# Kernel optimization log

Hardware: AMD Instinct MI355X
Metric: run time of the kernel (lower is better)

## Reference

```python
import jax, jax.numpy as jnp
import numpy as np

N_NODES, N_EDGES, D_IN, N_GRAPHS = 20000, 320000, 256, 32
H1, C1, H2, C2 = 4, 128, 4, 64


def setup_inputs() -> dict:
    key = jax.random.key(0)
    ks = jax.random.split(key, 24)
    g = lambda k, shape, fan: jax.random.normal(k, shape, jnp.float32) * (1.0 / np.sqrt(fan))
    inp = {
        'x': jax.random.normal(ks[0], (N_NODES, D_IN), jnp.float32),
        'edge_index': jax.random.randint(ks[1], (2, N_EDGES), 0, N_NODES, jnp.int32),
        'batch': jnp.sort(jax.random.randint(ks[2], (N_NODES,), 0, N_GRAPHS, jnp.int32)),
        'edge_attr': jax.random.normal(ks[3], (N_EDGES, 1), jnp.float32),
        # GATConv 1: lin [D_IN, H1*C1], att_src/dst/edge [H1,C1], lin_edge [1,H1*C1], bias [H1*C1]
        'W1': g(ks[4], (D_IN, H1 * C1), D_IN),
        'as1': g(ks[5], (H1, C1), C1),
        'ad1': g(ks[6], (H1, C1), C1),
        'We1': g(ks[7], (1, H1 * C1), 1),
        'ae1': g(ks[8], (H1, C1), C1),
        'b1': jnp.zeros((H1 * C1,), jnp.float32),
        'g1': jnp.ones((H1 * C1,), jnp.float32),
        'be1': jnp.zeros((H1 * C1,), jnp.float32),
        # GATConv 2 (concat=False -> out 64)
        'W2': g(ks[9], (H1 * C1, H2 * C2), H1 * C1),
        'as2': g(ks[10], (H2, C2), C2),
        'ad2': g(ks[11], (H2, C2), C2),
        'We2': g(ks[12], (1, H2 * C2), 1),
        'ae2': g(ks[13], (H2, C2), C2),
        'b2': jnp.zeros((C2,), jnp.float32),
        'g2': jnp.ones((C2,), jnp.float32),
        'be2': jnp.zeros((C2,), jnp.float32),
        'fw1': g(ks[14], (C2, 32), C2),
        'fb1': jnp.zeros((32,), jnp.float32),
        'fw2': g(ks[15], (32, 1), 32),
        'fb2': jnp.zeros((1,), jnp.float32),
    }
    return inp


def _gat(x, src, dst, ea, W, a_s, a_d, We, a_e, bias, H, C, concat, n):
    h = (x @ W).reshape(n, H, C)                         # [N,H,C]
    al_s = jnp.einsum('nhc,hc->nh', h, a_s)              # [N,H]
    al_d = jnp.einsum('nhc,hc->nh', h, a_d)
    e = (ea @ We).reshape(-1, H, C)                      # [E',H,C]
    al_e = jnp.einsum('ehc,hc->eh', e, a_e)
    logits = jax.nn.leaky_relu(al_s[src] + al_d[dst] + al_e, 0.2)  # [E',H]
    m = jax.ops.segment_max(logits, dst, num_segments=n)
    m = jnp.where(jnp.isfinite(m), m, 0.0)
    p = jnp.exp(logits - m[dst])
    denom = jax.ops.segment_sum(p, dst, num_segments=n)
    alpha = p / (denom[dst] + 1e-16)                     # segment softmax
    out = jax.ops.segment_sum(h[src] * alpha[:, :, None], dst, num_segments=n)
    out = out.reshape(n, H * C) if concat else out.mean(axis=1)
    return out + bias


def _bn(x, gamma, beta):
    mu = x.mean(axis=0)
    var = x.var(axis=0)
    return gamma * (x - mu) * jax.lax.rsqrt(var + 1e-5) + beta


def reference(x, edge_index, batch, edge_attr, W1, as1, ad1, We1, ae1, b1, g1, be1,
              W2, as2, ad2, We2, ae2, b2, g2, be2, fw1, fb1, fw2, fb2):
    n = x.shape[0]
    loop = jnp.arange(n, dtype=edge_index.dtype)
    src = jnp.concatenate([edge_index[0], loop])
    dst = jnp.concatenate([edge_index[1], loop])
    # self-loop edge_attr filled with mean (PyG fill_value='mean')
    ea = jnp.concatenate([edge_attr, jnp.broadcast_to(edge_attr.mean(axis=0), (n, edge_attr.shape[1]))])

    h = _gat(x, src, dst, ea, W1, as1, ad1, We1, ae1, b1, H1, C1, True, n)
    h = jax.nn.elu(_bn(h, g1, be1))
    h = _gat(h, src, dst, ea, W2, as2, ad2, We2, ae2, b2, H2, C2, False, n)
    h = jax.nn.elu(_bn(h, g2, be2))

    sums = jax.ops.segment_sum(h, batch, num_segments=N_GRAPHS)
    cnt = jax.ops.segment_sum(jnp.ones((n,), h.dtype), batch, num_segments=N_GRAPHS)
    pooled = sums / jnp.maximum(cnt, 1.0)[:, None]       # global_mean_pool
    # dropout is identity in eval mode
    out = jax.nn.elu(pooled @ fw1 + fb1) @ fw2 + fb2
    return out
```

## Files before the change

### kernel.cpp

```cpp
#include <hip/hip_runtime.h>
#include <hip/hip_bf16.h>

#define N_NODES  20000
#define MPAD     20096
#define N_EDGES  320000
#define N_EP     (N_EDGES + N_NODES)
#define D_IN     256
#define N_GRAPHS 32
#define HH1 4
#define CC1 128
#define HH2 4
#define CC2 64
#define MAXDEG   128

#define XB_OFF      0ull
#define HB1_OFF     10289152ull
#define AGG1_OFF    30867456ull
#define HB2_OFF     51445760ull
#define OUT2_OFF    61734912ull
#define EAF_OFF     66854912ull
#define W1BT_OFF    68134912ull
#define W2BT_OFF    68397056ull
#define CSR_OFF     68659200ull
#define ROWPTR_OFF  71379200ull
#define GSTART_OFF  71459264ull
#define SMALL_OFF   71459520ull
#define SBUF_OFF    71485120ull
#define EAP_OFF     71485184ull
#define ALSP_OFF    71486464ull
#define ALDP_OFF    72129536ull
#define PMU1_OFF    72772608ull
#define PM21_OFF    73296896ull
#define PMU2_OFF    73821184ull
#define PM22_OFF    73886720ull
#define A1_OFF      73952256ull
#define B1_OFF      73954304ull
#define A2_OFF      73956352ull
#define B2_OFF      73956608ull
#define EAACC_OFF   73956864ull
#define ALS_OFF     73956928ull
#define ALD_OFF     74278464ull
#define DEG_OFF     74600000ull
#define CURS_OFF    74680000ull
#define FLAGZ_OFF   74760000ull
#define ZERO0_START DEG_OFF
#define ZERO0_SIZE  160128ull
#define PP_OFF      74760128ull

#define S_AS1 0
#define S_AD1 512
#define S_WE1 1024
#define S_AE1 1536
#define S_G1  2048
#define S_BE1 2560
#define S_AS2 3072
#define S_AD2 3328
#define S_WE2 3584
#define S_AE2 3840
#define S_G2  4096
#define S_BE2 4160
#define S_FW1 4224
#define S_FB1 6272
#define S_FW2 6304
#define S_FB2 6336

typedef __attribute__((ext_vector_type(8))) short bf8_t;
typedef __attribute__((ext_vector_type(4))) float f4_t;

__global__ void detect_dtype(const unsigned short* __restrict__ xr, int* __restrict__ flag) {
    int i = blockIdx.x * blockDim.x + threadIdx.x;
    unsigned short u = xr[i];
    if ((u & 0x7F80) == 0x7F80) atomicOr(flag, 1);
}

__device__ __forceinline__ float loadF(const void* p, int i, int fp32) {
    return fp32 ? ((const float*)p)[i]
                : __bfloat162float(((const __hip_bfloat16*)p)[i]);
}

#define PB_XB  5024
#define PB_EAF 313
#define PB_W   512
#define PB_SM  16
#define PREP_BLOCKS (PB_XB + PB_EAF + 2 * PB_W + PB_SM + 1)
__global__ __launch_bounds__(256) void prep(
        const int* __restrict__ flag,
        const void* x, const void* ea, const void* W1, const void* W2,
        const void* as1, const void* ad1, const void* We1, const void* ae1,
        const void* g1, const void* be1, const void* as2, const void* ad2,
        const void* We2, const void* ae2, const void* g2, const void* be2,
        const void* fw1, const void* fb1, const void* fw2, const void* fb2,
        __hip_bfloat16* __restrict__ xb, float* __restrict__ eaf, float* __restrict__ eap,
        __hip_bfloat16* __restrict__ W1bt, __hip_bfloat16* __restrict__ W2bt,
        float* __restrict__ smalls, float* __restrict__ sbuf) {
    __shared__ float sh[256];
    int b = blockIdx.x, t = threadIdx.x;
    int fp32 = flag[0];
    if (b < PB_XB) {
        int base = (b * 256 + t) * 4;
        __hip_bfloat16 tmp[4];
#pragma unroll
        for (int j = 0; j < 4; ++j) {
            int i = base + j;
            float v = (i < N_NODES * D_IN) ? loadF(x, i, fp32) : 0.f;
            tmp[j] = __float2bfloat16(v);
        }
        *(uint2*)&xb[base] = *(uint2*)tmp;
        return;
    }
    b -= PB_XB;
    if (b < PB_EAF) {
        int base = (b * 256 + t) * 4;
        float s = 0.f;
#pragma unroll
        for (int j = 0; j < 4; ++j) {
            int i = base + j;
            if (i < N_EDGES) { float v = loadF(ea, i, fp32); eaf[i] = v; s += v; }
        }
        sh[t] = s;
        __syncthreads();
        for (int st = 128; st; st >>= 1) {
            if (t < st) sh[t] += sh[t + st];
            __syncthreads();
        }
        if (t == 0) eap[b] = sh[0];
        return;
    }
    b -= PB_EAF;
    if (b < PB_W) {
        int i = b * 256 + t;
        int k = i >> 9, n = i & 511;
        W1bt[(size_t)n * 256 + k] = __float2bfloat16(loadF(W1, i, fp32));
        return;
    }
    b -= PB_W;
    if (b < PB_W) {
        int i = b * 256 + t;
        int k = i >> 8, n = i & 255;
        W2bt[(size_t)n * 512 + k] = __float2bfloat16(loadF(W2, i, fp32));
        return;
    }
    b -= PB_W;
    if (b < PB_SM) {
        const void* srcs[16] = {as1, ad1, We1, ae1, g1, be1, as2, ad2, We2, ae2, g2, be2, fw1, fb1, fw2, fb2};
        const int cnts[16] = {512, 512, 512, 512, 512, 512, 256, 256, 256, 256, 64, 64, 2048, 32, 32, 1};
        const int offs[16] = {S_AS1, S_AD1, S_WE1, S_AE1, S_G1, S_BE1, S_AS2, S_AD2,
                              S_WE2, S_AE2, S_G2, S_BE2, S_FW1, S_FB1, S_FW2, S_FB2};
        for (int i = t; i < cnts[b]; i += 256)
            smalls[offs[b] + i] = loadF(srcs[b], i, fp32);
        return;
    }
    if (t < 4) {
        float s = 0.f;
        for (int c = 0; c < CC1; ++c) s += loadF(We1, t * CC1 + c, fp32) * loadF(ae1, t * CC1 + c, fp32);
        sbuf[t] = s;
    } else if (t < 8) {
        int h = t - 4;
        float s = 0.f;
        for (int c = 0; c < CC2; ++c) s += loadF(We2, h * CC2 + c, fp32) * loadF(ae2, h * CC2 + c, fp32);
        sbuf[4 + h] = s;
    }
}

#define HIST_BLOCKS 1329
__global__ void hist_bounds(const int* __restrict__ ei, int* __restrict__ deg,
                            const int* __restrict__ batch, int* __restrict__ gstart) {
    int b = blockIdx.x, t = threadIdx.x;
    if (b < HIST_BLOCKS) {
        int e = b * 256 + t;
        if (e >= N_EP) return;
        int d = (e < N_EDGES) ? ei[N_EDGES + e] : e - N_EDGES;
        atomicAdd(&deg[d], 1);
        return;
    }
    int i = (b - HIST_BLOCKS) * 256 + t;
    if (i >= N_NODES) return;
    int bb = batch[i];
    if (i == 0) {
        for (int g = 0; g <= bb; ++g) gstart[g] = 0;
    } else {
        int pb = batch[i - 1];
        for (int g = pb + 1; g <= bb; ++g) gstart[g] = i;
    }
    if (i == N_NODES - 1) {
        for (int g = bb + 1; g <= N_GRAPHS; ++g) gstart[g] = N_NODES;
    }
}

__global__ __launch_bounds__(1024) void deg_scan(const int* __restrict__ deg, int* __restrict__ rowptr,
                                                 const float* __restrict__ eap, float* __restrict__ ea_acc) {
    __shared__ int part[1024];
    int t = threadIdx.x;
    int lo = t * 20;
    int hi = lo + 20; if (hi > N_NODES) hi = N_NODES; if (lo > N_NODES) lo = N_NODES;
    int s = 0;
    for (int i = lo; i < hi; ++i) s += deg[i];
    part[t] = s;
    __syncthreads();
    for (int off = 1; off < 1024; off <<= 1) {
        int u = (t >= off) ? part[t - off] : 0;
        __syncthreads();
        if (t >= off) part[t] += u;
        __syncthreads();
    }
    int run = part[t] - s;
    for (int i = lo; i < hi; ++i) { rowptr[i] = run; run += deg[i]; }
    if (hi == N_NODES && lo < N_NODES) rowptr[N_NODES] = run;
    if (t == 0) {
        float es = 0.f;
        for (int i = 0; i < PB_EAF; ++i) es += eap[i];
        ea_acc[0] = es;
    }
}

__global__ void edge_scatter(const int* __restrict__ ei, const int* __restrict__ rowptr,
                             int* __restrict__ cursor, int2* __restrict__ csr_se) {
    int e = blockIdx.x * blockDim.x + threadIdx.x;
    if (e >= N_EP) return;
    int s, d;
    if (e < N_EDGES) { s = ei[e]; d = ei[N_EDGES + e]; }
    else { s = d = e - N_EDGES; }
    int pos = rowptr[d] + atomicAdd(&cursor[d], 1);
    csr_se[pos] = make_int2(s, e);
}

__global__ __launch_bounds__(64) void csr_sort(const int* __restrict__ rowptr, int2* __restrict__ cs) {
    __shared__ int2 buf[128];
    int d = blockIdx.x;
    int beg = rowptr[d], end = rowptr[d + 1], n = end - beg;
    int lane = threadIdx.x;
    if (n <= 1) return;
    if (n <= 128) {
        for (int i = lane; i < n; i += 64) buf[i] = cs[beg + i];
        __syncthreads();
        if (lane == 0) {
            for (int i = 1; i < n; ++i) {
                int2 key = buf[i]; int j = i - 1;
                while (j >= 0 && buf[j].y > key.y) { buf[j + 1] = buf[j]; --j; }
                buf[j + 1] = key;
            }
        }
        __syncthreads();
        for (int i = lane; i < n; i += 64) cs[beg + i] = buf[i];
    } else if (lane == 0) {
        for (int i = beg + 1; i < end; ++i) {
            int2 key = cs[i]; int j = i - 1;
            while (j >= beg && cs[j].y > key.y) { cs[j + 1] = cs[j]; --j; }
            cs[j + 1] = key;
        }
    }
}

__global__ __launch_bounds__(256) void gemm_mfma_al(
        const short* __restrict__ A, const short* __restrict__ Bt,
        __hip_bfloat16* __restrict__ Cb, int N, int K,
        float* __restrict__ alsp, float* __restrict__ aldp,
        const float* __restrict__ asv, const float* __restrict__ adv, int cshift) {
    __shared__ short As[128 * 40];
    __shared__ short Bs[64 * 40];
    int t = threadIdx.x;
    int wv = t >> 6, lane = t & 63, quad = lane >> 4, lr = lane & 15;
    int m0 = blockIdx.y * 128, n0 = blockIdx.x * 64;
    f4_t acc[2][4] = {};
    int ra0 = t >> 2, sa0 = t & 3;
    int ra1 = (t + 256) >> 2;
    for (int k0 = 0; k0 < K; k0 += 32) {
        *(uint4*)&As[ra0 * 40 + sa0 * 8] = *(const uint4*)&A[(size_t)(m0 + ra0) * K + k0 + sa0 * 8];
        *(uint4*)&As[ra1 * 40 + sa0 * 8] = *(const uint4*)&A[(size_t)(m0 + ra1) * K + k0 + sa0 * 8];
        *(uint4*)&Bs[ra0 * 40 + sa0 * 8] = *(const uint4*)&Bt[(size_t)(n0 + ra0) * K + k0 + sa0 * 8];
        __syncthreads();
        bf8_t a0 = *(const bf8_t*)&As[(wv * 16 + lr) * 40 + quad * 8];
        bf8_t a1 = *(const bf8_t*)&As[((wv + 4) * 16 + lr) * 40 + quad * 8];
#pragma unroll
        for (int nt = 0; nt < 4; ++nt) {
            bf8_t b = *(const bf8_t*)&Bs[(nt * 16 + lr) * 40 + quad * 8];
            acc[0][nt] = __builtin_amdgcn_mfma_f32_16x16x32_bf16(a0, b, acc[0][nt], 0, 0, 0);
            acc[1][nt] = __builtin_amdgcn_mfma_f32_16x16x32_bf16(a1, b, acc[1][nt], 0, 0, 0);
        }
        __syncthreads();
    }
#pragma unroll
    for (int si = 0; si < 2; ++si) {
        int mrow = m0 + (wv + si * 4) * 16 + quad * 4;
#pragma unroll
        for (int nt = 0; nt < 4; ++nt) {
            int col = n0 + nt * 16 + lr;
#pragma unroll
            for (int r = 0; r < 4; ++r)
                Cb[(size_t)(mrow + r) * N + col] = __float2bfloat16(acc[si][nt][r]);
        }
    }
    float asv4[4], adv4[4];
#pragma unroll
    for (int nt = 0; nt < 4; ++nt) {
        asv4[nt] = asv[n0 + nt * 16 + lr];
        adv4[nt] = adv[n0 + nt * 16 + lr];
    }
    int hsel = n0 >> cshift;
    int parity = (n0 >> 6) & ((1 << (cshift - 6)) - 1);
#pragma unroll
    for (int si = 0; si < 2; ++si) {
#pragma unroll
        for (int r = 0; r < 4; ++r) {
            float ps = 0.f, pd = 0.f;
#pragma unroll
            for (int nt = 0; nt < 4; ++nt) {
                ps += acc[si][nt][r] * asv4[nt];
                pd += acc[si][nt][r] * adv4[nt];
            }
#pragma unroll
            for (int m = 1; m < 16; m <<= 1) {
                ps += __shfl_xor(ps, m);
                pd += __shfl_xor(pd, m);
            }
            if (lr == 0) {
                int row = m0 + (wv + si * 4) * 16 + quad * 4 + r;
                alsp[(row * 4 + hsel) * 2 + parity] = ps;
                aldp[(row * 4 + hsel) * 2 + parity] = pd;
            }
        }
    }
}

__global__ void al_combine(const float* __restrict__ alsp, const float* __restrict__ aldp,
                           float* __restrict__ als, float* __restrict__ ald, int nparts) {
    int i = blockIdx.x * blockDim.x + threadIdx.x;
    if (i >= MPAD * 4) return;
    float s = alsp[2 * i], d0 = aldp[2 * i];
    if (nparts == 2) { s += alsp[2 * i + 1]; d0 += aldp[2 * i + 1]; }
    als[i] = s; ald[i] = d0;
}

__global__ __launch_bounds__(128) void fused_agg1(
        const int* __restrict__ rowptr, const int2* __restrict__ cs,
        const float* __restrict__ als, const float* __restrict__ ald,
        const float* __restrict__ eaf, const float* __restrict__ ea_acc,
        const float* __restrict__ sbuf, const __hip_bfloat16* __restrict__ hb,
        __hip_bfloat16* __restrict__ outb) {
    __shared__ float lg[MAXDEG * 4];
    __shared__ int   ssrc[MAXDEG];
    __shared__ float red[4 * 128];
    __shared__ float mxs[4], dns[4];
    int d = blockIdx.x, t = threadIdx.x;
    int beg = rowptr[d], end = rowptr[d + 1], n = end - beg;
    bool fit = (n <= MAXDEG);
    float ea_mean = ea_acc[0] * (1.0f / N_EDGES);
    float4 adv = *(const float4*)&ald[d * 4];
    float adh[4] = {adv.x, adv.y, adv.z, adv.w};
    float sb[4] = {sbuf[0], sbuf[1], sbuf[2], sbuf[3]};
    float mx[4] = {-INFINITY, -INFINITY, -INFINITY, -INFINITY};
    for (int p = t; p < n; p += 128) {
        int2 se = cs[beg + p];
        float eav = (se.y < N_EDGES) ? eaf[se.y] : ea_mean;
        float4 as = *(const float4*)&als[se.x * 4];
        float as4[4] = {as.x, as.y, as.z, as.w};
#pragma unroll
        for (int h = 0; h < 4; ++h) {
            float l = as4[h] + adh[h] + eav * sb[h];
            l = l > 0.f ? l : 0.2f * l;
            if (fit) lg[p * 4 + h] = l;
            mx[h] = fmaxf(mx[h], l);
        }
        if (fit) ssrc[p] = se.x;
    }
#pragma unroll
    for (int i = 0; i < 4; ++i) red[i * 128 + t] = mx[i];
    __syncthreads();
    for (int s = 64; s; s >>= 1) {
        if (t < s) {
#pragma unroll
            for (int i = 0; i < 4; ++i)
                red[i * 128 + t] = fmaxf(red[i * 128 + t], red[i * 128 + t + s]);
        }
        __syncthreads();
    }
    if (t < 4) mxs[t] = red[t * 128];
    __syncthreads();
    float m4[4] = {mxs[0], mxs[1], mxs[2], mxs[3]};
    float sm[4] = {0.f, 0.f, 0.f, 0.f};
    if (fit) {
        for (int p = t; p < n; p += 128) {
            float4 lv = *(float4*)&lg[p * 4];
            lv.x = __expf(lv.x - m4[0]); lv.y = __expf(lv.y - m4[1]);
            lv.z = __expf(lv.z - m4[2]); lv.w = __expf(lv.w - m4[3]);
            *(float4*)&lg[p * 4] = lv;
            sm[0] += lv.x; sm[1] += lv.y; sm[2] += lv.z; sm[3] += lv.w;
        }
    } else {
        for (int p = t; p < n; p += 128) {
            int2 se = cs[beg + p];
            float eav = (se.y < N_EDGES) ? eaf[se.y] : ea_mean;
            float4 as = *(const float4*)&als[se.x * 4];
            float as4[4] = {as.x, as.y, as.z, as.w};
#pragma unroll
            for (int h = 0; h < 4; ++h) {
                float l = as4[h] + adh[h] + eav * sb[h];
                l = l > 0.f ? l : 0.2f * l;
                sm[h] += __expf(l - m4[h]);
            }
        }
    }
    __syncthreads();
#pragma unroll
    for (int i = 0; i < 4; ++i) red[i * 128 + t] = sm[i];
    __syncthreads();
    for (int s = 64; s; s >>= 1) {
        if (t < s) {
#pragma unroll
            for (int i = 0; i < 4; ++i)
                red[i * 128 + t] += red[i * 128 + t + s];
        }
        __syncthreads();
    }
    if (t < 4) dns[t] = red[t * 128];
    __syncthreads();
    int h = t >> 5;
    float rdn = 1.0f / (dns[h] + 1e-16f);
    float a0 = 0.f, a1 = 0.f, a2 = 0.f, a3 = 0.f;
    if (fit) {
        for (int p = 0; p < n; ++p) {
            float w = lg[p * 4 + h];
            uint2 raw = *(const uint2*)&hb[(size_t)ssrc[p] * 512 + 4 * t];
            a0 += w * __uint_as_float(raw.x << 16);
            a1 += w * __uint_as_float(raw.x & 0xFFFF0000u);
            a2 += w * __uint_as_float(raw.y << 16);
            a3 += w * __uint_as_float(raw.y & 0xFFFF0000u);
        }
    } else {
        for (int p = 0; p < n; ++p) {
            int2 se = cs[beg + p];
            float eav = (se.y < N_EDGES) ? eaf[se.y] : ea_mean;
            float l = als[se.x * 4 + h] + adh[h] + eav * sb[h];
            l = l > 0.f ? l : 0.2f * l;
            float w = __expf(l - m4[h]);
            uint2 raw = *(const uint2*)&hb[(size_t)se.x * 512 + 4 * t];
            a0 += w * __uint_as_float(raw.x << 16);
            a1 += w * __uint_as_float(raw.x & 0xFFFF0000u);
            a2 += w * __uint_as_float(raw.y << 16);
            a3 += w * __uint_as_float(raw.y & 0xFFFF0000u);
        }
    }
    __hip_bfloat16 tmp[4] = {__float2bfloat16(a0 * rdn), __float2bfloat16(a1 * rdn),
                             __float2bfloat16(a2 * rdn), __float2bfloat16(a3 * rdn)};
    *(uint2*)&outb[(size_t)d * 512 + 4 * t] = *(uint2*)tmp;
}

__global__ __launch_bounds__(64) void fused_agg2(
        const int* __restrict__ rowptr, const int2* __restrict__ cs,
        const float* __restrict__ als, const float* __restrict__ ald,
        const float* __restrict__ eaf, const float* __restrict__ ea_acc,
        const float* __restrict__ sbuf, const __hip_bfloat16* __restrict__ hb,
        float* __restrict__ out2) {
    __shared__ float lg[MAXDEG * 4];
    __shared__ int   ssrc[MAXDEG];
    __shared__ float red[4 * 64];
    __shared__ float mxs[4], dns[4];
    __shared__ float shm[256];
    int d = blockIdx.x, t = threadIdx.x;
    int beg = rowptr[d], end = rowptr[d + 1], n = end - beg;
    bool fit = (n <= MAXDEG);
    float ea_mean = ea_acc[0] * (1.0f / N_EDGES);
    float4 adv = *(const float4*)&ald[d * 4];
    float adh[4] = {adv.x, adv.y, adv.z, adv.w};
    float sb[4] = {sbuf[4], sbuf[5], sbuf[6], sbuf[7]};
    float mx[4] = {-INFINITY, -INFINITY, -INFINITY, -INFINITY};
    for (int p = t; p < n; p += 64) {
        int2 se = cs[beg + p];
        float eav = (se.y < N_EDGES) ? eaf[se.y] : ea_mean;
        float4 as = *(const float4*)&als[se.x * 4];
        float as4[4] = {as.x, as.y, as.z, as.w};
#pragma unroll
        for (int h = 0; h < 4; ++h) {
            float l = as4[h] + adh[h] + eav * sb[h];
            l = l > 0.f ? l : 0.2f * l;
            if (fit) lg[p * 4 + h] = l;
            mx[h] = fmaxf(mx[h], l);
        }
        if (fit) ssrc[p] = se.x;
    }
#pragma unroll
    for (int i = 0; i < 4; ++i) red[i * 64 + t] = mx[i];
    __syncthreads();
    for (int s = 32; s; s >>= 1) {
        if (t < s) {
#pragma unroll
            for (int i = 0; i < 4; ++i)
                red[i * 64 + t] = fmaxf(red[i * 64 + t], red[i * 64 + t + s]);
        }
        __syncthreads();
    }
    if (t < 4) mxs[t] = red[t * 64];
    __syncthreads();
    float m4[4] = {mxs[0], mxs[1], mxs[2], mxs[3]};
    float sm[4] = {0.f, 0.f, 0.f, 0.f};
    if (fit) {
        for (int p = t; p < n; p += 64) {
            float4 lv = *(float4*)&lg[p * 4];
            lv.x = __expf(lv.x - m4[0]); lv.y = __expf(lv.y - m4[1]);
            lv.z = __expf(lv.z - m4[2]); lv.w = __expf(lv.w - m4[3]);
            *(float4*)&lg[p * 4] = lv;
            sm[0] += lv.x; sm[1] += lv.y; sm[2] += lv.z; sm[3] += lv.w;
        }
    } else {
        for (int p = t; p < n; p += 64) {
            int2 se = cs[beg + p];
            float eav = (se.y < N_EDGES) ? eaf[se.y] : ea_mean;
            float4 as = *(const float4*)&als[se.x * 4];
            float as4[4] = {as.x, as.y, as.z, as.w};
#pragma unroll
            for (int h = 0; h < 4; ++h) {
                float l = as4[h] + adh[h] + eav * sb[h];
                l = l > 0.f ? l : 0.2f * l;
                sm[h] += __expf(l - m4[h]);
            }
        }
    }
    __syncthreads();
#pragma unroll
    for (int i = 0; i < 4; ++i) red[i * 64 + t] = sm[i];
    __syncthreads();
    for (int s = 32; s; s >>= 1) {
        if (t < s) {
#pragma unroll
            for (int i = 0; i < 4; ++i)
                red[i * 64 + t] += red[i * 64 + t + s];
        }
        __syncthreads();
    }
    if (t < 4) dns[t] = red[t * 64];
    __syncthreads();
    int h = t >> 4;
    float rdn = 1.0f / (dns[h] + 1e-16f);
    float a0 = 0.f, a1 = 0.f, a2 = 0.f, a3 = 0.f;
    if (fit) {
        for (int p = 0; p < n; ++p) {
            float w = lg[p * 4 + h];
            uint2 raw = *(const uint2*)&hb[(size_t)ssrc[p] * 256 + 4 * t];
            a0 += w * __uint_as_float(raw.x << 16);
            a1 += w * __uint_as_float(raw.x & 0xFFFF0000u);
            a2 += w * __uint_as_float(raw.y << 16);
            a3 += w * __uint_as_float(raw.y & 0xFFFF0000u);
        }
    } else {
        for (int p = 0; p < n; ++p) {
            int2 se = cs[beg + p];
            float eav = (se.y < N_EDGES) ? eaf[se.y] : ea_mean;
            float l = als[se.x * 4 + h] + adh[h] + eav * sb[h];
            l = l > 0.f ? l : 0.2f * l;
            float w = __expf(l - m4[h]);
            uint2 raw = *(const uint2*)&hb[(size_t)se.x * 256 + 4 * t];
            a0 += w * __uint_as_float(raw.x << 16);
            a1 += w * __uint_as_float(raw.x & 0xFFFF0000u);
            a2 += w * __uint_as_float(raw.y << 16);
            a3 += w * __uint_as_float(raw.y & 0xFFFF0000u);
        }
    }
    shm[4 * t] = a0 * rdn; shm[4 * t + 1] = a1 * rdn;
    shm[4 * t + 2] = a2 * rdn; shm[4 * t + 3] = a3 * rdn;
    __syncthreads();
    if (t < 16) {
        float4 v;
        v.x = 0.25f * (shm[4 * t] + shm[64 + 4 * t] + shm[128 + 4 * t] + shm[192 + 4 * t]);
        v.y = 0.25f * (shm[4 * t + 1] + shm[64 + 4 * t + 1] + shm[128 + 4 * t + 1] + shm[192 + 4 * t + 1]);
        v.z = 0.25f * (shm[4 * t + 2] + shm[64 + 4 * t + 2] + shm[128 + 4 * t + 2] + shm[192 + 4 * t + 2]);
        v.w = 0.25f * (shm[4 * t + 3] + shm[64 + 4 * t + 3] + shm[128 + 4 * t + 3] + shm[192 + 4 * t + 3]);
        *(float4*)&out2[(size_t)d * 64 + 4 * t] = v;
    }
}

__global__ __launch_bounds__(256) void bn_part_b(const __hip_bfloat16* __restrict__ x,
                                                 float* __restrict__ pmu, float* __restrict__ pm2) {
    int t = threadIdx.x, b = blockIdx.x;
    float s0 = 0.f, s20 = 0.f, s1 = 0.f, s21 = 0.f;
    for (int i = b; i < N_NODES; i += gridDim.x) {
        unsigned u = *(const unsigned*)&x[(size_t)i * 512 + 2 * t];
        float v0 = __uint_as_float(u << 16);
        float v1 = __uint_as_float(u & 0xFFFF0000u);
        s0 += v0; s20 += v0 * v0; s1 += v1; s21 += v1 * v1;
    }
    pmu[b * 512 + 2 * t] = s0;     pm2[b * 512 + 2 * t] = s20;
    pmu[b * 512 + 2 * t + 1] = s1; pm2[b * 512 + 2 * t + 1] = s21;
}

__global__ void bn_reduce_affine(const float* __restrict__ pmu, const float* __restrict__ pm2,
                                 const float* __restrict__ smalls, int s_g, int s_be,
                                 float* __restrict__ a, float* __restrict__ b, int nch) {
    int c = blockIdx.x * blockDim.x + threadIdx.x;
    if (c >= nch) return;
    float s = 0.f, s2 = 0.f;
    for (int bk = 0; bk < 256; ++bk) { s += pmu[bk * nch + c]; s2 += pm2[bk * nch + c]; }
    float m = s * (1.0f / N_NODES);
    float var = s2 * (1.0f / N_NODES) - m * m;
    float aa = smalls[s_g + c] * rsqrtf(var + 1e-5f);
    a[c] = aa;
    b[c] = smalls[s_be + c] - m * aa;
}

__global__ __launch_bounds__(256) void bn_apply_elu_b16(__hip_bfloat16* __restrict__ x,
                                                        const float* __restrict__ a,
                                                        const float* __restrict__ b) {
    int q = blockIdx.x * blockDim.x + threadIdx.x;
    if (q >= N_NODES * 512 / 4) return;
    int base = q * 4;
    int j = base & 511;
    uint2 raw = *(uint2*)&x[base];
    float v[4] = {__uint_as_float(raw.x << 16), __uint_as_float(raw.x & 0xFFFF0000u),
                  __uint_as_float(raw.y << 16), __uint_as_float(raw.y & 0xFFFF0000u)};
    __hip_bfloat16 tmp[4];
#pragma unroll
    for (int k = 0; k < 4; ++k) {
        float y = a[j + k] * v[k] + b[j + k];
        y = y > 0.f ? y : expm1f(y);
        tmp[k] = __float2bfloat16(y);
    }
    *(uint2*)&x[base] = *(uint2*)tmp;
}

__global__ __launch_bounds__(256) void bn2_stats(const float* __restrict__ x,
                                                 float* __restrict__ pmu, float* __restrict__ pm2) {
    int t = threadIdx.x;
    int c = t & 63, j = t >> 6;
    float ls = 0.f, ls2 = 0.f;
    for (int nd = blockIdx.x * 4 + j; nd < N_NODES; nd += gridDim.x * 4) {
        float v = x[(size_t)nd * 64 + c];
        ls += v; ls2 += v * v;
    }
    __shared__ float shs[4][64], sh2[4][64];
    shs[j][c] = ls; sh2[j][c] = ls2;
    __syncthreads();
    if (j == 0) {
        pmu[blockIdx.x * 64 + c] = shs[0][c] + shs[1][c] + shs[2][c] + shs[3][c];
        pm2[blockIdx.x * 64 + c] = sh2[0][c] + sh2[1][c] + sh2[2][c] + sh2[3][c];
    }
}

__global__ __launch_bounds__(256) void pool_part(const float* __restrict__ x, const int* __restrict__ gstart,
                                                 const float* __restrict__ a2, const float* __restrict__ b2,
                                                 float* __restrict__ pp) {
    int g = blockIdx.x >> 3, ck = blockIdx.x & 7;
    int t = threadIdx.x;
    int c = t & 63, j = t >> 6;
    int beg = gstart[g], end = gstart[g + 1], n = end - beg;
    int cb = beg + (n * ck) / 8, ce = beg + (n * (ck + 1)) / 8;
    float ac = a2[c], bc = b2[c];
    float s = 0.f;
    for (int i = cb + j; i < ce; i += 4) {
        float y = ac * x[(size_t)i * 64 + c] + bc;
        s += (y > 0.f ? y : expm1f(y));
    }
    __shared__ float sh[4][64];
    sh[j][c] = s;
    __syncthreads();
    if (j == 0)
        pp[blockIdx.x * 64 + c] = sh[0][c] + sh[1][c] + sh[2][c] + sh[3][c];
}

__global__ __launch_bounds__(64) void pool_mlp_fin(const float* __restrict__ pp, const int* __restrict__ gstart,
                                                   const float* __restrict__ smalls, const int* __restrict__ flag,
                                                   void* __restrict__ outp) {
    int g = blockIdx.x, t = threadIdx.x;
    __shared__ float pooled[64];
    __shared__ float hsh[32];
    float s = 0.f;
    for (int k = 0; k < 8; ++k) s += pp[(g * 8 + k) * 64 + t];
    int n = gstart[g + 1] - gstart[g];
    pooled[t] = s / fmaxf((float)n, 1.0f);
    __syncthreads();
    if (t < 32) {
        float acc = smalls[S_FB1 + t];
        for (int cc = 0; cc < 64; ++cc)
            acc += pooled[cc] * smalls[S_FW1 + cc * 32 + t];
        hsh[t] = acc > 0.f ? acc : expm1f(acc);
    }
    __syncthreads();
    if (t == 0) {
        float o = smalls[S_FB2];
        for (int k = 0; k < 32; ++k) o += hsh[k] * smalls[S_FW2 + k];
        if (flag[0]) ((float*)outp)[g] = o;
        else ((__hip_bfloat16*)outp)[g] = __float2bfloat16(o);
    }
}

extern "C" void kernel_launch(void* const* d_in, const int* in_sizes, int n_in,
                              void* d_out, int out_size, void* d_ws, size_t ws_size,
                              hipStream_t stream) {
    const void* x    = d_in[0];
    const int* ei    = (const int*)d_in[1];
    const int* batch = (const int*)d_in[2];
    const void* ea   = d_in[3];
    const void* W1   = d_in[4];
    const void* as1  = d_in[5];
    const void* ad1  = d_in[6];
    const void* We1  = d_in[7];
    const void* ae1  = d_in[8];
    const void* g1   = d_in[10];
    const void* be1  = d_in[11];
    const void* W2   = d_in[12];
    const void* as2  = d_in[13];
    const void* ad2  = d_in[14];
    const void* We2  = d_in[15];
    const void* ae2  = d_in[16];
    const void* g2   = d_in[18];
    const void* be2  = d_in[19];
    const void* fw1  = d_in[20];
    const void* fb1  = d_in[21];
    const void* fw2  = d_in[22];
    const void* fb2  = d_in[23];

    char* ws = (char*)d_ws;
    __hip_bfloat16* xb   = (__hip_bfloat16*)(ws + XB_OFF);
    __hip_bfloat16* hb1  = (__hip_bfloat16*)(ws + HB1_OFF);
    __hip_bfloat16* agg1 = (__hip_bfloat16*)(ws + AGG1_OFF);
    __hip_bfloat16* hb2  = (__hip_bfloat16*)(ws + HB2_OFF);
    float* out2   = (float*)(ws + OUT2_OFF);
    float* eaf    = (float*)(ws + EAF_OFF);
    __hip_bfloat16* W1bt = (__hip_bfloat16*)(ws + W1BT_OFF);
    __hip_bfloat16* W2bt = (__hip_bfloat16*)(ws + W2BT_OFF);
    int2*  csr_se = (int2*)(ws + CSR_OFF);
    int*   rowptr = (int*)(ws + ROWPTR_OFF);
    int*   gstart = (int*)(ws + GSTART_OFF);
    float* smalls = (float*)(ws + SMALL_OFF);
    float* sbuf   = (float*)(ws + SBUF_OFF);
    float* eap    = (float*)(ws + EAP_OFF);
    float* alsp   = (float*)(ws + ALSP_OFF);
    float* aldp   = (float*)(ws + ALDP_OFF);
    float* pmu1   = (float*)(ws + PMU1_OFF);
    float* pm21   = (float*)(ws + PM21_OFF);
    float* pmu2   = (float*)(ws + PMU2_OFF);
    float* pm22   = (float*)(ws + PM22_OFF);
    float* a1     = (float*)(ws + A1_OFF);
    float* b1     = (float*)(ws + B1_OFF);
    float* a2     = (float*)(ws + A2_OFF);
    float* b2     = (float*)(ws + B2_OFF);
    float* ea_acc = (float*)(ws + EAACC_OFF);
    float* als    = (float*)(ws + ALS_OFF);
    float* ald    = (float*)(ws + ALD_OFF);
    float* pp     = (float*)(ws + PP_OFF);
    int*   deg    = (int*)(ws + DEG_OFF);
    int*   cursor = (int*)(ws + CURS_OFF);
    int*   flag   = (int*)(ws + FLAGZ_OFF);

    hipMemsetAsync(ws + ZERO0_START, 0, ZERO0_SIZE, stream);
    hipMemsetAsync(ws + AGG1_OFF + (size_t)N_NODES * 512 * 2, 0, (MPAD - N_NODES) * 512 * 2, stream);

    detect_dtype<<<256, 256, 0, stream>>>((const unsigned short*)x, flag);
    prep<<<PREP_BLOCKS, 256, 0, stream>>>(flag, x, ea, W1, W2,
                                          as1, ad1, We1, ae1, g1, be1, as2, ad2,
                                          We2, ae2, g2, be2, fw1, fb1, fw2, fb2,
                                          xb, eaf, eap, W1bt, W2bt, smalls, sbuf);

    hist_bounds<<<HIST_BLOCKS + 79, 256, 0, stream>>>(ei, deg, batch, gstart);
    deg_scan<<<1, 1024, 0, stream>>>(deg, rowptr, eap, ea_acc);
    edge_scatter<<<HIST_BLOCKS, 256, 0, stream>>>(ei, rowptr, cursor, csr_se);
    csr_sort<<<N_NODES, 64, 0, stream>>>(rowptr, csr_se);

    gemm_mfma_al<<<dim3(512 / 64, MPAD / 128), 256, 0, stream>>>(
        (const short*)xb, (const short*)W1bt, hb1, 512, 256,
        alsp, aldp, smalls + S_AS1, smalls + S_AD1, 7);
    al_combine<<<(MPAD * 4 + 255) / 256, 256, 0, stream>>>(alsp, aldp, als, ald, 2);
    fused_agg1<<<N_NODES, 128, 0, stream>>>(rowptr, csr_se, als, ald, eaf, ea_acc, sbuf, hb1, agg1);
    bn_part_b<<<256, 256, 0, stream>>>(agg1, pmu1, pm21);
    bn_reduce_affine<<<2, 256, 0, stream>>>(pmu1, pm21, smalls, S_G1, S_BE1, a1, b1, 512);
    bn_apply_elu_b16<<<10000, 256, 0, stream>>>(agg1, a1, b1);

    gemm_mfma_al<<<dim3(256 / 64, MPAD / 128), 256, 0, stream>>>(
        (const short*)agg1, (const short*)W2bt, hb2, 256, 512,
        alsp, aldp, smalls + S_AS2, smalls + S_AD2, 6);
    al_combine<<<(MPAD * 4 + 255) / 256, 256, 0, stream>>>(alsp, aldp, als, ald, 1);
    fused_agg2<<<N_NODES, 64, 0, stream>>>(rowptr, csr_se, als, ald, eaf, ea_acc, sbuf, hb2, out2);
    bn2_stats<<<256, 256, 0, stream>>>(out2, pmu2, pm22);
    bn_reduce_affine<<<1, 64, 0, stream>>>(pmu2, pm22, smalls, S_G2, S_BE2, a2, b2, 64);

    pool_part<<<N_GRAPHS * 8, 256, 0, stream>>>(out2, gstart, a2, b2, pp);
    pool_mlp_fin<<<N_GRAPHS, 64, 0, stream>>>(pp, gstart, smalls, flag, d_out);
}
```

Before: 443.3 us.

## Fuse BN1+ELU into second GEMM A-load and prebake edge attrs into CSR

Removes the standalone BN-apply/ELU pass over the layer-1 aggregate by applying the affine and ELU while loading A tiles in the second MFMA GEMM. A new csr_fill kernel overwrites the CSR edge-id field with the edge attribute value (or the self-loop mean), so both aggregation kernels skip the indirect eaf lookup. This trades a full read/write pass and gathers for redundant ELU computation across GEMM column blocks and an extra small kernel launch.

```diff
diff --git a/kernel.cpp b/kernel.cpp
--- a/kernel.cpp
+++ b/kernel.cpp
@@ -251,11 +251,22 @@
     }
 }
 
+__global__ void csr_fill(int2* __restrict__ cs, const float* __restrict__ eaf,
+                         const float* __restrict__ ea_acc) {
+    int p = blockIdx.x * blockDim.x + threadIdx.x;
+    if (p >= N_EP) return;
+    int e = cs[p].y;
+    float eav = (e < N_EDGES) ? eaf[e] : ea_acc[0] * (1.0f / N_EDGES);
+    cs[p].y = __float_as_int(eav);
+}
+
+template <bool BNA>
 __global__ __launch_bounds__(256) void gemm_mfma_al(
         const short* __restrict__ A, const short* __restrict__ Bt,
         __hip_bfloat16* __restrict__ Cb, int N, int K,
         float* __restrict__ alsp, float* __restrict__ aldp,
-        const float* __restrict__ asv, const float* __restrict__ adv, int cshift) {
+        const float* __restrict__ asv, const float* __restrict__ adv, int cshift,
+        const float* __restrict__ a1, const float* __restrict__ b1) {
     __shared__ short As[128 * 40];
     __shared__ short Bs[64 * 40];
     int t = threadIdx.x;
@@ -265,17 +276,48 @@
     int ra0 = t >> 2, sa0 = t & 3;
     int ra1 = (t + 256) >> 2;
     for (int k0 = 0; k0 < K; k0 += 32) {
-        *(uint4*)&As[ra0 * 40 + sa0 * 8] = *(const uint4*)&A[(size_t)(m0 + ra0) * K + k0 + sa0 * 8];
-        *(uint4*)&As[ra1 * 40 + sa0 * 8] = *(const uint4*)&A[(size_t)(m0 + ra1) * K + k0 + sa0 * 8];
+        int j0 = k0 + sa0 * 8;
+        {
+            uint4 raw = *(const uint4*)&A[(size_t)(m0 + ra0) * K + j0];
+            if (BNA) {
+                unsigned short us[8]; *(uint4*)us = raw;
+                __hip_bfloat16 ob[8];
+#pragma unroll
+                for (int i2 = 0; i2 < 8; ++i2) {
+                    float v = __uint_as_float(((unsigned)us[i2]) << 16);
+                    float y = a1[j0 + i2] * v + b1[j0 + i2];
+                    y = y > 0.f ? y : expm1f(y);
+                    ob[i2] = __float2bfloat16(y);
+                }
+                raw = *(uint4*)ob;
+            }
+            *(uint4*)&As[ra0 * 40 + sa0 * 8] = raw;
+        }
+        {
+            uint4 raw = *(const uint4*)&A[(size_t)(m0 + ra1) * K + j0];
+            if (BNA) {
+                unsigned short us[8]; *(uint4*)us = raw;
+                __hip_bfloat16 ob[8];
+#pragma unroll
+                for (int i2 = 0; i2 < 8; ++i2) {
+                    float v = __uint_as_float(((unsigned)us[i2]) << 16);
+                    float y = a1[j0 + i2] * v + b1[j0 + i2];
+                    y = y > 0.f ? y : expm1f(y);
+                    ob[i2] = __float2bfloat16(y);
+                }
+                raw = *(uint4*)ob;
+            }
+            *(uint4*)&As[ra1 * 40 + sa0 * 8] = raw;
+        }
         *(uint4*)&Bs[ra0 * 40 + sa0 * 8] = *(const uint4*)&Bt[(size_t)(n0 + ra0) * K + k0 + sa0 * 8];
         __syncthreads();
         bf8_t a0 = *(const bf8_t*)&As[(wv * 16 + lr) * 40 + quad * 8];
-        bf8_t a1 = *(const bf8_t*)&As[((wv + 4) * 16 + lr) * 40 + quad * 8];
+        bf8_t a1f = *(const bf8_t*)&As[((wv + 4) * 16 + lr) * 40 + quad * 8];
 #pragma unroll
         for (int nt = 0; nt < 4; ++nt) {
             bf8_t b = *(const bf8_t*)&Bs[(nt * 16 + lr) * 40 + quad * 8];
             acc[0][nt] = __builtin_amdgcn_mfma_f32_16x16x32_bf16(a0, b, acc[0][nt], 0, 0, 0);
-            acc[1][nt] = __builtin_amdgcn_mfma_f32_16x16x32_bf16(a1, b, acc[1][nt], 0, 0, 0);
+            acc[1][nt] = __builtin_amdgcn_mfma_f32_16x16x32_bf16(a1f, b, acc[1][nt], 0, 0, 0);
         }
         __syncthreads();
     }
@@ -334,7 +376,6 @@
 __global__ __launch_bounds__(128) void fused_agg1(
         const int* __restrict__ rowptr, const int2* __restrict__ cs,
         const float* __restrict__ als, const float* __restrict__ ald,
-        const float* __restrict__ eaf, const float* __restrict__ ea_acc,
         const float* __restrict__ sbuf, const __hip_bfloat16* __restrict__ hb,
         __hip_bfloat16* __restrict__ outb) {
     __shared__ float lg[MAXDEG * 4];
@@ -344,14 +385,13 @@
     int d = blockIdx.x, t = threadIdx.x;
     int beg = rowptr[d], end = rowptr[d + 1], n = end - beg;
     bool fit = (n <= MAXDEG);
-    float ea_mean = ea_acc[0] * (1.0f / N_EDGES);
     float4 adv = *(const float4*)&ald[d * 4];
     float adh[4] = {adv.x, adv.y, adv.z, adv.w};
     float sb[4] = {sbuf[0], sbuf[1], sbuf[2], sbuf[3]};
     float mx[4] = {-INFINITY, -INFINITY, -INFINITY, -INFINITY};
     for (int p = t; p < n; p += 128) {
         int2 se = cs[beg + p];
-        float eav = (se.y < N_EDGES) ? eaf[se.y] : ea_mean;
+        float eav = __int_as_float(se.y);
         float4 as = *(const float4*)&als[se.x * 4];
         float as4[4] = {as.x, as.y, as.z, as.w};
 #pragma unroll
@@ -389,7 +429,7 @@
     } else {
         for (int p = t; p < n; p += 128) {
             int2 se = cs[beg + p];
-            float eav = (se.y < N_EDGES) ? eaf[se.y] : ea_mean;
+            float eav = __int_as_float(se.y);
             float4 as = *(const float4*)&als[se.x * 4];
             float as4[4] = {as.x, as.y, as.z, as.w};
 #pragma unroll
@@ -429,7 +469,7 @@
     } else {
         for (int p = 0; p < n; ++p) {
             int2 se = cs[beg + p];
-            float eav = (se.y < N_EDGES) ? eaf[se.y] : ea_mean;
+            float eav = __int_as_float(se.y);
             float l = als[se.x * 4 + h] + adh[h] + eav * sb[h];
             l = l > 0.f ? l : 0.2f * l;
             float w = __expf(l - m4[h]);
@@ -448,7 +488,6 @@
 __global__ __launch_bounds__(64) void fused_agg2(
         const int* __restrict__ rowptr, const int2* __restrict__ cs,
         const float* __restrict__ als, const float* __restrict__ ald,
-        const float* __restrict__ eaf, const float* __restrict__ ea_acc,
         const float* __restrict__ sbuf, const __hip_bfloat16* __restrict__ hb,
         float* __restrict__ out2) {
     __shared__ float lg[MAXDEG * 4];
@@ -459,14 +498,13 @@
     int d = blockIdx.x, t = threadIdx.x;
     int beg = rowptr[d], end = rowptr[d + 1], n = end - beg;
     bool fit = (n <= MAXDEG);
-    float ea_mean = ea_acc[0] * (1.0f / N_EDGES);
     float4 adv = *(const float4*)&ald[d * 4];
     float adh[4] = {adv.x, adv.y, adv.z, adv.w};
     float sb[4] = {sbuf[4], sbuf[5], sbuf[6], sbuf[7]};
     float mx[4] = {-INFINITY, -INFINITY, -INFINITY, -INFINITY};
     for (int p = t; p < n; p += 64) {
         int2 se = cs[beg + p];
-        float eav = (se.y < N_EDGES) ? eaf[se.y] : ea_mean;
+        float eav = __int_as_float(se.y);
         float4 as = *(const float4*)&als[se.x * 4];
         float as4[4] = {as.x, as.y, as.z, as.w};
 #pragma unroll
@@ -504,7 +542,7 @@
     } else {
         for (int p = t; p < n; p += 64) {
             int2 se = cs[beg + p];
-            float eav = (se.y < N_EDGES) ? eaf[se.y] : ea_mean;
+            float eav = __int_as_float(se.y);
             float4 as = *(const float4*)&als[se.x * 4];
             float as4[4] = {as.x, as.y, as.z, as.w};
 #pragma unroll
@@ -544,7 +582,7 @@
     } else {
         for (int p = 0; p < n; ++p) {
             int2 se = cs[beg + p];
-            float eav = (se.y < N_EDGES) ? eaf[se.y] : ea_mean;
+            float eav = __int_as_float(se.y);
             float l = als[se.x * 4 + h] + adh[h] + eav * sb[h];
             l = l > 0.f ? l : 0.2f * l;
             float w = __expf(l - m4[h]);
@@ -594,26 +632,6 @@
     float aa = smalls[s_g + c] * rsqrtf(var + 1e-5f);
     a[c] = aa;
     b[c] = smalls[s_be + c] - m * aa;
-}
-
-__global__ __launch_bounds__(256) void bn_apply_elu_b16(__hip_bfloat16* __restrict__ x,
-                                                        const float* __restrict__ a,
-                                                        const float* __restrict__ b) {
-    int q = blockIdx.x * blockDim.x + threadIdx.x;
-    if (q >= N_NODES * 512 / 4) return;
-    int base = q * 4;
-    int j = base & 511;
-    uint2 raw = *(uint2*)&x[base];
-    float v[4] = {__uint_as_float(raw.x << 16), __uint_as_float(raw.x & 0xFFFF0000u),
-                  __uint_as_float(raw.y << 16), __uint_as_float(raw.y & 0xFFFF0000u)};
-    __hip_bfloat16 tmp[4];
-#pragma unroll
-    for (int k = 0; k < 4; ++k) {
-        float y = a[j + k] * v[k] + b[j + k];
-        y = y > 0.f ? y : expm1f(y);
-        tmp[k] = __float2bfloat16(y);
-    }
-    *(uint2*)&x[base] = *(uint2*)tmp;
 }
 
 __global__ __launch_bounds__(256) void bn2_stats(const float* __restrict__ x,
@@ -753,21 +771,21 @@
     deg_scan<<<1, 1024, 0, stream>>>(deg, rowptr, eap, ea_acc);
     edge_scatter<<<HIST_BLOCKS, 256, 0, stream>>>(ei, rowptr, cursor, csr_se);
     csr_sort<<<N_NODES, 64, 0, stream>>>(rowptr, csr_se);
-
-    gemm_mfma_al<<<dim3(512 / 64, MPAD / 128), 256, 0, stream>>>(
+    csr_fill<<<HIST_BLOCKS, 256, 0, stream>>>(csr_se, eaf, ea_acc);
+
+    gemm_mfma_al<false><<<dim3(512 / 64, MPAD / 128), 256, 0, stream>>>(
         (const short*)xb, (const short*)W1bt, hb1, 512, 256,
-        alsp, aldp, smalls + S_AS1, smalls + S_AD1, 7);
+        alsp, aldp, smalls + S_AS1, smalls + S_AD1, 7, nullptr, nullptr);
     al_combine<<<(MPAD * 4 + 255) / 256, 256, 0, stream>>>(alsp, aldp, als, ald, 2);
-    fused_agg1<<<N_NODES, 128, 0, stream>>>(rowptr, csr_se, als, ald, eaf, ea_acc, sbuf, hb1, agg1);
+    fused_agg1<<<N_NODES, 128, 0, stream>>>(rowptr, csr_se, als, ald, sbuf, hb1, agg1);
     bn_part_b<<<256, 256, 0, stream>>>(agg1, pmu1, pm21);
     bn_reduce_affine<<<2, 256, 0, stream>>>(pmu1, pm21, smalls, S_G1, S_BE1, a1, b1, 512);
-    bn_apply_elu_b16<<<10000, 256, 0, stream>>>(agg1, a1, b1);
-
-    gemm_mfma_al<<<dim3(256 / 64, MPAD / 128), 256, 0, stream>>>(
+
+    gemm_mfma_al<true><<<dim3(256 / 64, MPAD / 128), 256, 0, stream>>>(
         (const short*)agg1, (const short*)W2bt, hb2, 256, 512,
-        alsp, aldp, smalls + S_AS2, smalls + S_AD2, 6);
+        alsp, aldp, smalls + S_AS2, smalls + S_AD2, 6, a1, b1);
     al_combine<<<(MPAD * 4 + 255) / 256, 256, 0, stream>>>(alsp, aldp, als, ald, 1);
-    fused_agg2<<<N_NODES, 64, 0, stream>>>(rowptr, csr_se, als, ald, eaf, ea_acc, sbuf, hb2, out2);
+    fused_agg2<<<N_NODES, 64, 0, stream>>>(rowptr, csr_se, als, ald, sbuf, hb2, out2);
     bn2_stats<<<256, 256, 0, stream>>>(out2, pmu2, pm22);
     bn_reduce_affine<<<1, 64, 0, stream>>>(pmu2, pm22, smalls, S_G2, S_BE2, a2, b2, 64);
 
```

Result: slower. 457.4 us (+3.2%).
